# Performance work log

Measured on AMD Instinct MI355X. Metric: run time of the kernel, lower is better.

## Reference

```python
import jax, jax.numpy as jnp
import numpy as np

N_USERS, N_ITEMS, DIM = 50000, 25000, 128
E_H, E_R = 600000, 1000000
N_LAYERS = 2


def setup_inputs() -> dict:
    key = jax.random.key(0)
    ks = jax.random.split(key, 20)
    nrm = lambda k, s: jax.random.normal(k, s, jnp.float32) * 0.05
    inp = {
        "u_emb": nrm(ks[0], (N_USERS, DIM)),
        "i_emb": nrm(ks[1], (N_ITEMS, DIM)),
        "gating_W": nrm(ks[2], (4, DIM, DIM)),
        "gating_b": jnp.zeros((4, DIM), jnp.float32),
        "attention": nrm(ks[3], (DIM,)),
        "attention_mat": nrm(ks[4], (DIM, DIM)),
    }
    for i, name in enumerate(["Hs", "Hj", "Hp"]):
        inp[name + "_row"] = jax.random.randint(ks[5 + 2 * i], (E_H,), 0, N_USERS, jnp.int32)
        inp[name + "_col"] = jax.random.randint(ks[6 + 2 * i], (E_H,), 0, N_USERS, jnp.int32)
        inp[name + "_val"] = jax.random.uniform(ks[11 + i], (E_H,), jnp.float32)
    inp["R_row"] = jax.random.randint(ks[14], (E_R,), 0, N_USERS, jnp.int32)
    inp["R_col"] = jax.random.randint(ks[15], (E_R,), 0, N_ITEMS, jnp.int32)
    inp["R_val"] = jnp.ones((E_R,), jnp.float32)
    return inp


def spmm(row, col, val, X, n_out):
    # sparse (n_out x n_in) @ dense (n_in x d), COO edge list form
    return jax.ops.segment_sum(val[:, None] * X[col], row, num_segments=n_out)


def l2norm(x):
    return x * jax.lax.rsqrt(jnp.maximum(jnp.sum(x * x, axis=1, keepdims=True), 1e-12))


def reference(u_emb, i_emb, gating_W, gating_b, attention, attention_mat,
              Hs_row, Hs_col, Hs_val, Hj_row, Hj_col, Hj_val,
              Hp_row, Hp_col, Hp_val, R_row, R_col, R_val):
    gate = lambda e, c: e * jax.nn.sigmoid(e @ gating_W[c] + gating_b[c])

    def chan_att(cs):
        # per-channel attention score: sum_d a_d * (E_c @ W_att)_d  -> [N, C]
        w = jnp.stack([jnp.sum(attention * (c @ attention_mat), axis=1) for c in cs], axis=1)
        s = jax.nn.softmax(w, axis=1)
        mixed = sum(s[:, k:k + 1] * cs[k] for k in range(len(cs)))
        return mixed, s

    H = [(Hs_row, Hs_col, Hs_val), (Hj_row, Hj_col, Hj_val), (Hp_row, Hp_col, Hp_val)]
    cur = [gate(u_emb, c) for c in range(3)]        # channel user embeddings
    cur_s = gate(u_emb, 3)                          # simple-gated user embeddings
    cur_i = i_emb
    all_c = [[cur[k]] for k in range(3)]
    all_i = [cur_i]
    all_s = [cur_s]
    for _ in range(N_LAYERS):
        mixed = chan_att(cur)[0] + cur_s / 2
        for k in range(3):
            r, c, v = H[k]
            cur[k] = spmm(r, c, v, cur[k], N_USERS)
            all_c[k].append(l2norm(cur[k]))
        new_item = spmm(R_col, R_row, R_val, mixed, N_ITEMS)   # R^T @ mixed
        all_i.append(l2norm(new_item))
        cur_s = spmm(R_row, R_col, R_val, cur_i, N_USERS)      # R @ item
        all_s.append(l2norm(cur_s))
        cur_i = new_item
    fc = [sum(all_c[k]) for k in range(3)]
    final_user = chan_att(fc)[0] + sum(all_s) / 2
    final_item = sum(all_i)
    return jnp.concatenate([final_user, final_item], axis=0)  # [N_USERS+N_ITEMS, DIM]
```

## Files before the change

kernel.cpp:

```cpp
#include <hip/hip_runtime.h>
#include <cstddef>
#include <cstdint>

#define NU 50000
#define NI 25000
#define DIMN 128
#define EH 600000
#define ER 1000000

typedef unsigned int u32;
typedef unsigned long long u64;
typedef unsigned char u8;
typedef __attribute__((ext_vector_type(8))) short short8;
typedef __attribute__((ext_vector_type(16))) float float16;

__device__ __forceinline__ float wave_sum64(float v) {
#pragma unroll
  for (int m = 32; m >= 1; m >>= 1) v += __shfl_xor(v, m, 64);
  return v;
}

__device__ __forceinline__ u32 pack_bf16x2(float a, float b) {
  u32 ua = __float_as_uint(a), ub = __float_as_uint(b);
  ua = (ua + 0x7fffu + ((ua >> 16) & 1u)) >> 16;
  ub = (ub + 0x7fffu + ((ub >> 16) & 1u)) >> 16;
  return ua | (ub << 16);
}
__device__ __forceinline__ u32 bf16_hi(float v) {
  u32 u = __float_as_uint(v);
  u = (u + 0x7fffu + ((u >> 16) & 1u)) & 0xffff0000u;
  return u;
}
__device__ __forceinline__ float blo(u32 p) { return __uint_as_float(p << 16); }
__device__ __forceinline__ float bhi(u32 p) { return __uint_as_float(p & 0xffff0000u); }

struct Graphs {
  const int* row[5];
  const int* col[5];
  const float* val[5];
};

__device__ __forceinline__ int g_E(int z) {
  const int E[5] = {EH, EH, EH, ER, ER};
  return E[z];
}

#define NBKU 196
#define TOTB (5 * NBKU)
#define CAPH 3584
#define CAPR 5632
#define CAPT 5632
#define ECAP 4315136
#define FCAP 5760
#define CHUNK 2048

#define BSH 293
#define BSR 489
#define B1SCAT (3 * BSH + 2 * BSR)
#define B1PREP 18879
#define B2FINE TOTB
#define B2GATE (782 * 4)

__device__ __forceinline__ int capstart(int z, int b) {
  const int base[5] = {0, 702464, 1404928, 2107392, 3211264};
  const int cap[5] = {CAPH, CAPH, CAPH, CAPR, CAPT};
  return base[z] + b * cap[z];
}

__global__ __launch_bounds__(256) void k_build1(Graphs g, int* __restrict__ bcnt,
                                                u32* __restrict__ epb, u8* __restrict__ erb,
                                                const float* __restrict__ U,
                                                u32* __restrict__ UP16,
                                                const float* __restrict__ IE,
                                                u32* __restrict__ IE16,
                                                const float* __restrict__ W,
                                                u32* __restrict__ W16,
                                                const float* __restrict__ attm,
                                                const float* __restrict__ att,
                                                float* __restrict__ attv) {
  int b = blockIdx.x;
  if (b < B1SCAT) {
    int z, cb;
    if (b < 3 * BSH) {
      z = b / BSH;
      cb = b - z * BSH;
    } else {
      int r = b - 3 * BSH;
      z = 3 + r / BSR;
      cb = r - (z - 3) * BSR;
    }
    int E = g_E(z);
    int sh = (z == 4) ? 7 : 8;
    int mask = (1 << sh) - 1;
    __shared__ int hist[2][NBKU], basel[NBKU], curl[2][NBKU], h0s[NBKU];
    for (int i = threadIdx.x; i < NBKU; i += 256) {
      hist[0][i] = 0;
      hist[1][i] = 0;
      curl[0][i] = 0;
      curl[1][i] = 0;
    }
    __syncthreads();
    const int* __restrict__ row = g.row[z];
    const int* __restrict__ col = g.col[z];
    const float* __restrict__ val = g.val[z];
    int e0 = cb * CHUNK + threadIdx.x * 8;
    int half = threadIdx.x >> 7;
    int r[8];
    u32 pay[8];
    bool ok[8];
    if (e0 + 8 <= E) {
      int4 ra = *(const int4*)(row + e0);
      int4 rb = *(const int4*)(row + e0 + 4);
      int4 ca = *(const int4*)(col + e0);
      int4 cbv = *(const int4*)(col + e0 + 4);
      r[0] = ra.x; r[1] = ra.y; r[2] = ra.z; r[3] = ra.w;
      r[4] = rb.x; r[5] = rb.y; r[6] = rb.z; r[7] = rb.w;
      pay[0] = (u32)ca.x; pay[1] = (u32)ca.y; pay[2] = (u32)ca.z; pay[3] = (u32)ca.w;
      pay[4] = (u32)cbv.x; pay[5] = (u32)cbv.y; pay[6] = (u32)cbv.z; pay[7] = (u32)cbv.w;
#pragma unroll
      for (int k = 0; k < 8; ++k) ok[k] = true;
      if (z < 3) {
        float4 va = *(const float4*)(val + e0);
        float4 vb = *(const float4*)(val + e0 + 4);
        pay[0] |= bf16_hi(va.x); pay[1] |= bf16_hi(va.y);
        pay[2] |= bf16_hi(va.z); pay[3] |= bf16_hi(va.w);
        pay[4] |= bf16_hi(vb.x); pay[5] |= bf16_hi(vb.y);
        pay[6] |= bf16_hi(vb.z); pay[7] |= bf16_hi(vb.w);
      }
    } else {
#pragma unroll
      for (int k = 0; k < 8; ++k) {
        int e = e0 + k;
        ok[k] = e < E;
        r[k] = ok[k] ? row[e] : 0;
        pay[k] = ok[k] ? (u32)col[e] : 0u;
        if (z < 3 && ok[k]) pay[k] |= bf16_hi(val[e]);
      }
    }
#pragma unroll
    for (int k = 0; k < 8; ++k)
      if (ok[k]) atomicAdd(&hist[half][r[k] >> sh], 1);
    __syncthreads();
    for (int i = threadIdx.x; i < NBKU; i += 256) {
      int h0 = hist[0][i];
      int tot = h0 + hist[1][i];
      h0s[i] = h0;
      if (tot) basel[i] = capstart(z, i) + atomicAdd(&bcnt[z * NBKU + i], tot);
    }
    __syncthreads();
#pragma unroll
    for (int k = 0; k < 8; ++k)
      if (ok[k]) {
        int bb = r[k] >> sh;
        int rank = atomicAdd(&curl[half][bb], 1);
        int pos = basel[bb] + (half ? h0s[bb] : 0) + rank;
        epb[pos] = pay[k];
        erb[pos] = (u8)(r[k] & mask);
      }
    return;
  }
  int b2 = b - B1SCAT;
  if (b2 < 12500) {
    int i = b2 * 256 + threadIdx.x;
    float2 v = ((const float2*)U)[i];
    UP16[i] = pack_bf16x2(v.x, v.y);
  } else if (b2 < 18750) {
    int i = (b2 - 12500) * 256 + threadIdx.x;
    float2 v = ((const float2*)IE)[i];
    IE16[i] = pack_bf16x2(v.x, v.y);
  } else if (b2 < 18878) {
    int i = (b2 - 18750) * 256 + threadIdx.x;
    int col = i & 127, k2 = (i >> 7) & 63, c = i >> 13;
    const float* Wc = W + (size_t)c * DIMN * DIMN;
    W16[i] = pack_bf16x2(Wc[(size_t)(2 * k2) * DIMN + col], Wc[(size_t)(2 * k2 + 1) * DIMN + col]);
  } else {
    int e = threadIdx.x;
    if (e < 128) {
      float s = 0.f;
      for (int d = 0; d < DIMN; ++d) s += attm[e * DIMN + d] * att[d];
      attv[e] = s;
    }
  }
}

struct FineLds {
  int cnt[256];
  int scn[256];
  int curl[256];
  u32 buf[FCAP];
};
struct GateLds {
  u32 ldsP[64 * 65];
};

__global__ __launch_bounds__(256) void k_build2(u32* __restrict__ epb, const u8* __restrict__ erb,
                                                const int* __restrict__ bcnt,
                                                int* __restrict__ ptr2,
                                                const u32* __restrict__ UP16,
                                                const u32* __restrict__ W16,
                                                const float* __restrict__ B, u32* S16,
                                                u32* G016, u32* G116, u32* G216) {
  __shared__ __align__(16) union {
    FineLds f;
    GateLds g;
  } sh;
  int b = blockIdx.x;
  int t = threadIdx.x;
  if (b < B2FINE) {
    int z = b / NBKU, bb = b - z * NBKU;
    int shf = (z == 4) ? 7 : 8;
    int mask = (1 << shf) - 1;
    const int poffs2[5] = {0, 100000, 200000, 300000, 400000};
    const int nz[5] = {NU, NU, NU, NU, NI};
    int s = capstart(z, bb);
    int n = bcnt[z * NBKU + bb];
    FineLds& L = sh.f;
    L.cnt[t] = 0;
    L.curl[t] = 0;
    __syncthreads();
    int n4 = n >> 2;
    for (int i = t; i < n4; i += 256) {
      u32 r4 = *(const u32*)(erb + s + 4 * i);
      atomicAdd(&L.cnt[r4 & 255u], 1);
      atomicAdd(&L.cnt[(r4 >> 8) & 255u], 1);
      atomicAdd(&L.cnt[(r4 >> 16) & 255u], 1);
      atomicAdd(&L.cnt[r4 >> 24], 1);
    }
    for (int i = 4 * n4 + t; i < n; i += 256) atomicAdd(&L.cnt[erb[s + i]], 1);
    __syncthreads();
    int v = L.cnt[t];
    L.scn[t] = v;
    __syncthreads();
    for (int o = 1; o < 256; o <<= 1) {
      int x = (t >= o) ? L.scn[t - o] : 0;
      __syncthreads();
      L.scn[t] += x;
      __syncthreads();
    }
    int excl = L.scn[t] - v;
    __syncthreads();
    L.scn[t] = excl;
    int rg = (bb << shf) + t;
    if (t <= mask && rg < nz[z]) {
      ptr2[poffs2[z] + 2 * rg] = s + excl;
      ptr2[poffs2[z] + 2 * rg + 1] = s + excl + v;
    }
    __syncthreads();
    for (int i = t; i < n4; i += 256) {
      u32 r4 = *(const u32*)(erb + s + 4 * i);
      uint4 p4 = *(const uint4*)(epb + s + 4 * i);
      int r0 = (int)(r4 & 255u);
      int k0 = atomicAdd(&L.curl[r0], 1);
      L.buf[L.scn[r0] + k0] = p4.x;
      int r1 = (int)((r4 >> 8) & 255u);
      int k1 = atomicAdd(&L.curl[r1], 1);
      L.buf[L.scn[r1] + k1] = p4.y;
      int r2 = (int)((r4 >> 16) & 255u);
      int k2 = atomicAdd(&L.curl[r2], 1);
      L.buf[L.scn[r2] + k2] = p4.z;
      int r3 = (int)(r4 >> 24);
      int k3 = atomicAdd(&L.curl[r3], 1);
      L.buf[L.scn[r3] + k3] = p4.w;
    }
    for (int i = 4 * n4 + t; i < n; i += 256) {
      int r = erb[s + i];
      int rank = atomicAdd(&L.curl[r], 1);
      L.buf[L.scn[r] + rank] = epb[s + i];
    }
    __syncthreads();
    for (int i = t; i < n4; i += 256) ((uint4*)(epb + s))[i] = ((const uint4*)L.buf)[i];
    for (int i = 4 * n4 + t; i < n; i += 256) epb[s + i] = L.buf[i];
    return;
  }
  int gb = b - B2FINE;
  int c = gb / 782;
  int r0 = (gb - c * 782) * 64;
  const u32* __restrict__ Wc = W16 + (size_t)c * (64 * 128);
  int w = t >> 6, lane = t & 63;
  int ln = lane & 31, h = lane >> 5;
  int rh = w & 1, mh = w >> 1;
  u32* ldsP = sh.g.ldsP;

  int rowl = rh * 32 + ln;
  int rg = r0 + rowl;
  int rc = (rg < NU) ? rg : (NU - 1);

  float16 acc[2];
#pragma unroll
  for (int m = 0; m < 2; ++m)
#pragma unroll
    for (int q = 0; q < 16; ++q) acc[m][q] = 0.f;

  const u32* __restrict__ urow = UP16 + (size_t)rc * 64;
#pragma unroll
  for (int kk = 0; kk < 8; ++kk) {
    int kw = kk * 8 + 4 * h;
    union {
      u32 u[4];
      short8 s;
    } bf;
#pragma unroll
    for (int j = 0; j < 4; ++j) bf.u[j] = urow[kw + j];
#pragma unroll
    for (int m = 0; m < 2; ++m) {
      union {
        u32 u[4];
        short8 s;
      } af;
      int col = 64 * mh + 32 * m + ln;
#pragma unroll
      for (int j = 0; j < 4; ++j) af.u[j] = Wc[(size_t)(kw + j) * DIMN + col];
      acc[m] = __builtin_amdgcn_mfma_f32_32x32x16_bf16(af.s, bf.s, acc[m], 0, 0, 0);
    }
  }
#pragma unroll
  for (int m = 0; m < 2; ++m)
#pragma unroll
    for (int q = 0; q < 16; q += 2) {
      int cw = 32 * mh + 16 * m + ((q & 3) >> 1) + 4 * (q >> 2) + 2 * h;
      ldsP[rowl * 65 + cw] = pack_bf16x2(acc[m][q], acc[m][q + 1]);
    }
  __syncthreads();

  int colw = t & 63, rloc = t >> 6;
  float bx = B[c * DIMN + 2 * colw], by = B[c * DIMN + 2 * colw + 1];
  u32* dst = (c == 0) ? G016 : (c == 1) ? G116 : (c == 2) ? G216 : S16;
#pragma unroll
  for (int i = 0; i < 16; ++i) {
    int row = i * 4 + rloc;
    int rg2 = r0 + row;
    if (rg2 >= NU) continue;
    u32 p = ldsP[row * 65 + colw];
    u32 uu = UP16[(size_t)rg2 * 64 + colw];
    float sx = 1.f / (1.f + __expf(-(blo(p) + bx)));
    float sy = 1.f / (1.f + __expf(-(bhi(p) + by)));
    dst[(size_t)rg2 * 64 + colw] = pack_bf16x2(blo(uu) * sx, bhi(uu) * sy);
  }
}

struct Job {
  const int* ptr2;
  const u32* X16;
  u32* Y16;
  float* ACCF;
  u32* ACC16;
  const u32* AINIT16;
  const float* AINITF;
  int nrows;
};

template <bool UNIT>
__device__ __forceinline__ void spmm_run(const u32* __restrict__ ep, const Job& jb) {
  int w = blockIdx.x * 4 + __builtin_amdgcn_readfirstlane(threadIdx.x >> 6);
  int lane = threadIdx.x & 63;
  if (w >= jb.nrows) return;
  const int2 pp = ((const int2*)jb.ptr2)[w];
  int s = __builtin_amdgcn_readfirstlane(pp.x);
  int t = __builtin_amdgcn_readfirstlane(pp.y);
  const char* __restrict__ Xb = (const char*)jb.X16;
  u32 lo4 = (u32)(lane << 2);
  float ax = 0.f, ay = 0.f;
  int e = s;
  for (; e + 8 <= t; e += 8) {
    u32 off[8];
    float vv[8];
#pragma unroll
    for (int k = 0; k < 8; ++k) {
      u32 q = ep[e + k];
      if (UNIT) {
        off[k] = (q << 8) | lo4;
      } else {
        off[k] = ((q & 0xffffu) << 8) | lo4;
        vv[k] = bhi(q);
      }
    }
    u32 p[8];
#pragma unroll
    for (int k = 0; k < 8; ++k) p[k] = *(const u32*)(Xb + off[k]);
#pragma unroll
    for (int k = 0; k < 8; ++k) {
      if (UNIT) {
        ax += blo(p[k]);
        ay += bhi(p[k]);
      } else {
        ax += vv[k] * blo(p[k]);
        ay += vv[k] * bhi(p[k]);
      }
    }
  }
  for (; e + 4 <= t; e += 4) {
    u32 off[4];
    float vv[4];
#pragma unroll
    for (int k = 0; k < 4; ++k) {
      u32 q = ep[e + k];
      if (UNIT) {
        off[k] = (q << 8) | lo4;
      } else {
        off[k] = ((q & 0xffffu) << 8) | lo4;
        vv[k] = bhi(q);
      }
    }
    u32 p[4];
#pragma unroll
    for (int k = 0; k < 4; ++k) p[k] = *(const u32*)(Xb + off[k]);
#pragma unroll
    for (int k = 0; k < 4; ++k) {
      if (UNIT) {
        ax += blo(p[k]);
        ay += bhi(p[k]);
      } else {
        ax += vv[k] * blo(p[k]);
        ay += vv[k] * bhi(p[k]);
      }
    }
  }
  for (; e < t; ++e) {
    u32 q = ep[e];
    u32 off;
    float v = 1.f;
    if (UNIT) {
      off = (q << 8) | lo4;
    } else {
      off = ((q & 0xffffu) << 8) | lo4;
      v = bhi(q);
    }
    u32 p = *(const u32*)(Xb + off);
    ax += v * blo(p);
    ay += v * bhi(p);
  }
  size_t b64 = (size_t)w * 64 + lane;
  if (jb.ACCF) {
    float ss = wave_sum64(ax * ax + ay * ay);
    float rs = rsqrtf(fmaxf(ss, 1e-12f));
    if (jb.Y16) jb.Y16[b64] = pack_bf16x2(ax, ay);
    float2 o;
    if (jb.AINITF)
      o = *(const float2*)(jb.AINITF + 2 * b64);
    else
      o = *(const float2*)(jb.ACCF + 2 * b64);
    o.x += ax * rs;
    o.y += ay * rs;
    *(float2*)(jb.ACCF + 2 * b64) = o;
  } else if (jb.ACC16) {
    float ss = wave_sum64(ax * ax + ay * ay);
    float rs = rsqrtf(fmaxf(ss, 1e-12f));
    u32 p = jb.AINIT16 ? jb.AINIT16[b64] : jb.ACC16[b64];
    float ox = blo(p) + ax * rs, oy = bhi(p) + ay * rs;
    if (jb.Y16) jb.Y16[b64] = pack_bf16x2(ax, ay);
    jb.ACC16[b64] = pack_bf16x2(ox, oy);
  } else if (jb.Y16) {
    jb.Y16[b64] = pack_bf16x2(ax, ay);
  }
}

__global__ __launch_bounds__(256) void k_spmm5(const u32* __restrict__ ep, Job j0, Job j1,
                                               Job j2, Job j3, Job j4) {
  int y = blockIdx.y;
  if (y < 2) {
    Job jb = (y == 0) ? j0 : j1;
    spmm_run<true>(ep, jb);
  } else {
    Job jb = (y == 2) ? j2 : (y == 3) ? j3 : j4;
    spmm_run<false>(ep, jb);
  }
}

template <bool OUT16>
__global__ __launch_bounds__(256) void k_mix(const u32* __restrict__ c0_,
                                             const u32* __restrict__ c1_,
                                             const u32* __restrict__ c2_,
                                             const u32* __restrict__ sp_,
                                             const float* __restrict__ attv, float* outf,
                                             u32* out16, int nrows) {
  int w = blockIdx.x * 4 + __builtin_amdgcn_readfirstlane(threadIdx.x >> 6);
  int lane = threadIdx.x & 63;
  if (w >= nrows) return;
  size_t b64 = (size_t)w * 64 + lane;
  u32 p0 = c0_[b64], p1 = c1_[b64], p2 = c2_[b64];
  float2 x0 = make_float2(blo(p0), bhi(p0));
  float2 x1 = make_float2(blo(p1), bhi(p1));
  float2 x2 = make_float2(blo(p2), bhi(p2));
  float2 av = *(const float2*)(attv + lane * 2);
  float w0 = wave_sum64(x0.x * av.x + x0.y * av.y);
  float w1 = wave_sum64(x1.x * av.x + x1.y * av.y);
  float w2 = wave_sum64(x2.x * av.x + x2.y * av.y);
  float m = fmaxf(w0, fmaxf(w1, w2));
  float e0 = __expf(w0 - m), e1 = __expf(w1 - m), e2 = __expf(w2 - m);
  float inv = 1.f / (e0 + e1 + e2);
  float s0 = e0 * inv, s1 = e1 * inv, s2 = e2 * inv;
  u32 ps = sp_[b64];
  float ox = s0 * x0.x + s1 * x1.x + s2 * x2.x + 0.5f * blo(ps);
  float oy = s0 * x0.y + s1 * x1.y + s2 * x2.y + 0.5f * bhi(ps);
  if (OUT16)
    out16[b64] = pack_bf16x2(ox, oy);
  else
    *(float2*)(outf + 2 * b64) = make_float2(ox, oy);
}

extern "C" void kernel_launch(void* const* d_in, const int* in_sizes, int n_in, void* d_out,
                              int out_size, void* d_ws, size_t ws_size, hipStream_t stream) {
  const float* u_emb = (const float*)d_in[0];
  const float* i_emb = (const float*)d_in[1];
  const float* gW = (const float*)d_in[2];
  const float* gB = (const float*)d_in[3];
  const float* att = (const float*)d_in[4];
  const float* attm = (const float*)d_in[5];
  Graphs g;
  g.row[0] = (const int*)d_in[6];
  g.col[0] = (const int*)d_in[7];
  g.val[0] = (const float*)d_in[8];
  g.row[1] = (const int*)d_in[9];
  g.col[1] = (const int*)d_in[10];
  g.val[1] = (const float*)d_in[11];
  g.row[2] = (const int*)d_in[12];
  g.col[2] = (const int*)d_in[13];
  g.val[2] = (const float*)d_in[14];
  g.row[3] = (const int*)d_in[15];
  g.col[3] = (const int*)d_in[16];
  g.val[3] = (const float*)d_in[17];
  g.row[4] = (const int*)d_in[16];
  g.col[4] = (const int*)d_in[15];
  g.val[4] = (const float*)d_in[17];

  const size_t U = (size_t)NU * DIMN, U64 = (size_t)NU * 64, I64 = (size_t)NI * 64;
  u32* G016 = (u32*)d_ws;
  u32* G116 = G016 + U64;
  u32* G216 = G116 + U64;
  u32* C1016 = G216 + U64;
  u32* C1116 = C1016 + U64;
  u32* C1216 = C1116 + U64;
  u32* GS016 = C1216 + U64;
  u32* GS116 = GS016 + U64;
  u32* GS216 = GS116 + U64;
  u32* MIX16 = GS216 + U64;
  u32* S16 = MIX16 + U64;
  u32* SACC = S16 + U64;
  u32* I116 = SACC + U64;
  u32* IE16 = I116 + I64;
  u32* UP16 = IE16 + I64;
  u32* W16 = UP16 + U64;
  float* attv = (float*)(W16 + 32768);
  int* ptr2 = (int*)(attv + DIMN);
  int* bcnt = ptr2 + 450000;
  uintptr_t a0 = ((uintptr_t)(bcnt + 984) + 15u) & ~(uintptr_t)15;
  u32* epb = (u32*)a0;
  u8* erb = (u8*)(epb + ECAP);
  float* out_u = (float*)d_out;
  float* out_i = out_u + U;

  const int GRID_U = (NU + 3) / 4;
  const int po1 = 100000, po2 = 200000, po3 = 300000, po4 = 400000;

  hipMemsetAsync(bcnt, 0, TOTB * sizeof(int), stream);
  hipLaunchKernelGGL(k_build1, dim3(B1SCAT + B1PREP), dim3(256), 0, stream, g, bcnt, epb, erb,
                     u_emb, UP16, i_emb, IE16, gW, W16, attm, att, attv);
  hipLaunchKernelGGL(k_build2, dim3(B2FINE + B2GATE), dim3(256), 0, stream, epb, erb, bcnt, ptr2,
                     UP16, W16, gB, S16, G016, G116, G216);

  hipLaunchKernelGGL((k_mix<true>), dim3(GRID_U), dim3(256), 0, stream, G016, G116, G216, S16,
                     attv, (float*)nullptr, MIX16, NU);
  {
    Job j0 = {ptr2 + po3, IE16, S16, nullptr, SACC, S16, nullptr, NU};
    Job j1 = {ptr2 + po4, MIX16, I116, out_i, nullptr, nullptr, i_emb, NI};
    Job j2 = {ptr2, G016, C1016, nullptr, GS016, G016, nullptr, NU};
    Job j3 = {ptr2 + po1, G116, C1116, nullptr, GS116, G116, nullptr, NU};
    Job j4 = {ptr2 + po2, G216, C1216, nullptr, GS216, G216, nullptr, NU};
    hipLaunchKernelGGL(k_spmm5, dim3(GRID_U, 5), dim3(256), 0, stream, epb, j0, j1, j2, j3, j4);
  }

  hipLaunchKernelGGL((k_mix<true>), dim3(GRID_U), dim3(256), 0, stream, C1016, C1116, C1216, S16,
                     attv, (float*)nullptr, MIX16, NU);
  {
    Job j0 = {ptr2 + po3, I116, nullptr, nullptr, SACC, nullptr, nullptr, NU};
    Job j1 = {ptr2 + po4, MIX16, nullptr, out_i, nullptr, nullptr, nullptr, NI};
    Job j2 = {ptr2, C1016, nullptr, nullptr, GS016, nullptr, nullptr, NU};
    Job j3 = {ptr2 + po1, C1116, nullptr, nullptr, GS116, nullptr, nullptr, NU};
    Job j4 = {ptr2 + po2, C1216, nullptr, nullptr, GS216, nullptr, nullptr, NU};
    hipLaunchKernelGGL(k_spmm5, dim3(GRID_U, 5), dim3(256), 0, stream, epb, j0, j1, j2, j3, j4);
  }

  hipLaunchKernelGGL((k_mix<false>), dim3(GRID_U), dim3(256), 0, stream, GS016, GS116, GS216,
                     SACC, attv, out_u, (u32*)nullptr, NU);
}
```

Baseline: 495.2 us.

## Fuse four gating channels and channel-attention mix into build2 with vectorized bf16 prep

```diff
diff --git a/kernel.cpp b/kernel.cpp
--- a/kernel.cpp
+++ b/kernel.cpp
@@ -57,9 +57,12 @@
 #define BSH 293
 #define BSR 489
 #define B1SCAT (3 * BSH + 2 * BSR)
-#define B1PREP 18879
+#define PU 3125
+#define PIE 1563
+#define PW 128
+#define B1PREP (PU + PIE + PW + 1)
 #define B2FINE TOTB
-#define B2GATE (782 * 4)
+#define B2GATE 782
 
 __device__ __forceinline__ int capstart(int z, int b) {
   const int base[5] = {0, 702464, 1404928, 2107392, 3211264};
@@ -160,16 +163,30 @@
     return;
   }
   int b2 = b - B1SCAT;
-  if (b2 < 12500) {
+  if (b2 < PU) {
     int i = b2 * 256 + threadIdx.x;
-    float2 v = ((const float2*)U)[i];
-    UP16[i] = pack_bf16x2(v.x, v.y);
-  } else if (b2 < 18750) {
-    int i = (b2 - 12500) * 256 + threadIdx.x;
-    float2 v = ((const float2*)IE)[i];
-    IE16[i] = pack_bf16x2(v.x, v.y);
-  } else if (b2 < 18878) {
-    int i = (b2 - 18750) * 256 + threadIdx.x;
+    float4 a = ((const float4*)U)[2 * i];
+    float4 c = ((const float4*)U)[2 * i + 1];
+    uint4 o;
+    o.x = pack_bf16x2(a.x, a.y);
+    o.y = pack_bf16x2(a.z, a.w);
+    o.z = pack_bf16x2(c.x, c.y);
+    o.w = pack_bf16x2(c.z, c.w);
+    ((uint4*)UP16)[i] = o;
+  } else if (b2 < PU + PIE) {
+    int i = (b2 - PU) * 256 + threadIdx.x;
+    if (i < (NI * DIMN) / 8) {
+      float4 a = ((const float4*)IE)[2 * i];
+      float4 c = ((const float4*)IE)[2 * i + 1];
+      uint4 o;
+      o.x = pack_bf16x2(a.x, a.y);
+      o.y = pack_bf16x2(a.z, a.w);
+      o.z = pack_bf16x2(c.x, c.y);
+      o.w = pack_bf16x2(c.z, c.w);
+      ((uint4*)IE16)[i] = o;
+    }
+  } else if (b2 < PU + PIE + PW) {
+    int i = (b2 - PU - PIE) * 256 + threadIdx.x;
     int col = i & 127, k2 = (i >> 7) & 63, c = i >> 13;
     const float* Wc = W + (size_t)c * DIMN * DIMN;
     W16[i] = pack_bf16x2(Wc[(size_t)(2 * k2) * DIMN + col], Wc[(size_t)(2 * k2 + 1) * DIMN + col]);
@@ -184,22 +201,27 @@
 }
 
 struct FineLds {
-  int cnt[256];
-  int scn[256];
-  int curl[256];
+  int cnt[1024];
+  int scn[1024];
+  int curl[1024];
   u32 buf[FCAP];
 };
 struct GateLds {
-  u32 ldsP[64 * 65];
+  u32 ldsP[4][64 * 64];
 };
 
-__global__ __launch_bounds__(256) void k_build2(u32* __restrict__ epb, const u8* __restrict__ erb,
-                                                const int* __restrict__ bcnt,
-                                                int* __restrict__ ptr2,
-                                                const u32* __restrict__ UP16,
-                                                const u32* __restrict__ W16,
-                                                const float* __restrict__ B, u32* S16,
-                                                u32* G016, u32* G116, u32* G216) {
+__device__ __forceinline__ int gsw(int row, int col) { return row * 64 + (col ^ (row & 31)); }
+
+__global__ __launch_bounds__(1024) void k_build2(u32* __restrict__ epb,
+                                                 const u8* __restrict__ erb,
+                                                 const int* __restrict__ bcnt,
+                                                 int* __restrict__ ptr2,
+                                                 const u32* __restrict__ UP16,
+                                                 const u32* __restrict__ W16,
+                                                 const float* __restrict__ B,
+                                                 const float* __restrict__ attv, u32* S16,
+                                                 u32* G016, u32* G116, u32* G216,
+                                                 u32* MIX16) {
   __shared__ __align__(16) union {
     FineLds f;
     GateLds g;
@@ -219,14 +241,14 @@
     L.curl[t] = 0;
     __syncthreads();
     int n4 = n >> 2;
-    for (int i = t; i < n4; i += 256) {
+    for (int i = t; i < n4; i += 1024) {
       u32 r4 = *(const u32*)(erb + s + 4 * i);
       atomicAdd(&L.cnt[r4 & 255u], 1);
       atomicAdd(&L.cnt[(r4 >> 8) & 255u], 1);
       atomicAdd(&L.cnt[(r4 >> 16) & 255u], 1);
       atomicAdd(&L.cnt[r4 >> 24], 1);
     }
-    for (int i = 4 * n4 + t; i < n; i += 256) atomicAdd(&L.cnt[erb[s + i]], 1);
+    for (int i = 4 * n4 + t; i < n; i += 1024) atomicAdd(&L.cnt[erb[s + i]], 1);
     __syncthreads();
     int v = L.cnt[t];
     L.scn[t] = v;
@@ -246,7 +268,7 @@
       ptr2[poffs2[z] + 2 * rg + 1] = s + excl + v;
     }
     __syncthreads();
-    for (int i = t; i < n4; i += 256) {
+    for (int i = t; i < n4; i += 1024) {
       u32 r4 = *(const u32*)(erb + s + 4 * i);
       uint4 p4 = *(const uint4*)(epb + s + 4 * i);
       int r0 = (int)(r4 & 255u);
@@ -262,24 +284,26 @@
       int k3 = atomicAdd(&L.curl[r3], 1);
       L.buf[L.scn[r3] + k3] = p4.w;
     }
-    for (int i = 4 * n4 + t; i < n; i += 256) {
+    for (int i = 4 * n4 + t; i < n; i += 1024) {
       int r = erb[s + i];
       int rank = atomicAdd(&L.curl[r], 1);
       L.buf[L.scn[r] + rank] = epb[s + i];
     }
     __syncthreads();
-    for (int i = t; i < n4; i += 256) ((uint4*)(epb + s))[i] = ((const uint4*)L.buf)[i];
-    for (int i = 4 * n4 + t; i < n; i += 256) epb[s + i] = L.buf[i];
+    for (int i = t; i < n4; i += 1024) ((uint4*)(epb + s))[i] = ((const uint4*)L.buf)[i];
+    for (int i = 4 * n4 + t; i < n; i += 1024) epb[s + i] = L.buf[i];
     return;
   }
   int gb = b - B2FINE;
-  int c = gb / 782;
-  int r0 = (gb - c * 782) * 64;
-  const u32* __restrict__ Wc = W16 + (size_t)c * (64 * 128);
-  int w = t >> 6, lane = t & 63;
+  int r0 = gb * 64;
+  int wv = t >> 6;
+  int c = wv >> 2;
+  int w = wv & 3;
+  int lane = t & 63;
   int ln = lane & 31, h = lane >> 5;
   int rh = w & 1, mh = w >> 1;
-  u32* ldsP = sh.g.ldsP;
+  const u32* __restrict__ Wc = W16 + (size_t)c * (64 * 128);
+  u32* ldsP = sh.g.ldsP[c];
 
   int rowl = rh * 32 + ln;
   int rg = r0 + rowl;
@@ -318,23 +342,53 @@
 #pragma unroll
     for (int q = 0; q < 16; q += 2) {
       int cw = 32 * mh + 16 * m + ((q & 3) >> 1) + 4 * (q >> 2) + 2 * h;
-      ldsP[rowl * 65 + cw] = pack_bf16x2(acc[m][q], acc[m][q + 1]);
+      ldsP[gsw(rowl, cw)] = pack_bf16x2(acc[m][q], acc[m][q + 1]);
     }
   __syncthreads();
 
-  int colw = t & 63, rloc = t >> 6;
-  float bx = B[c * DIMN + 2 * colw], by = B[c * DIMN + 2 * colw + 1];
-  u32* dst = (c == 0) ? G016 : (c == 1) ? G116 : (c == 2) ? G216 : S16;
-#pragma unroll
-  for (int i = 0; i < 16; ++i) {
-    int row = i * 4 + rloc;
+  int colw = lane;
+  float2 av = *(const float2*)(attv + 2 * colw);
+  float2 b0 = ((const float2*)B)[colw];
+  float2 b1 = ((const float2*)B)[64 + colw];
+  float2 b2 = ((const float2*)B)[128 + colw];
+  float2 b3 = ((const float2*)B)[192 + colw];
+#pragma unroll
+  for (int i = 0; i < 4; ++i) {
+    int row = wv + i * 16;
     int rg2 = r0 + row;
     if (rg2 >= NU) continue;
-    u32 p = ldsP[row * 65 + colw];
-    u32 uu = UP16[(size_t)rg2 * 64 + colw];
-    float sx = 1.f / (1.f + __expf(-(blo(p) + bx)));
-    float sy = 1.f / (1.f + __expf(-(bhi(p) + by)));
-    dst[(size_t)rg2 * 64 + colw] = pack_bf16x2(blo(uu) * sx, bhi(uu) * sy);
+    size_t o64 = (size_t)rg2 * 64 + colw;
+    u32 uu = UP16[o64];
+    float ux = blo(uu), uy = bhi(uu);
+    u32 p0 = sh.g.ldsP[0][gsw(row, colw)];
+    u32 p1 = sh.g.ldsP[1][gsw(row, colw)];
+    u32 p2 = sh.g.ldsP[2][gsw(row, colw)];
+    u32 p3 = sh.g.ldsP[3][gsw(row, colw)];
+    u32 g0 = pack_bf16x2(ux / (1.f + __expf(-(blo(p0) + b0.x))),
+                         uy / (1.f + __expf(-(bhi(p0) + b0.y))));
+    u32 g1 = pack_bf16x2(ux / (1.f + __expf(-(blo(p1) + b1.x))),
+                         uy / (1.f + __expf(-(bhi(p1) + b1.y))));
+    u32 g2 = pack_bf16x2(ux / (1.f + __expf(-(blo(p2) + b2.x))),
+                         uy / (1.f + __expf(-(bhi(p2) + b2.y))));
+    u32 g3 = pack_bf16x2(ux / (1.f + __expf(-(blo(p3) + b3.x))),
+                         uy / (1.f + __expf(-(bhi(p3) + b3.y))));
+    G016[o64] = g0;
+    G116[o64] = g1;
+    G216[o64] = g2;
+    S16[o64] = g3;
+    float x0x = blo(g0), x0y = bhi(g0);
+    float x1x = blo(g1), x1y = bhi(g1);
+    float x2x = blo(g2), x2y = bhi(g2);
+    float w0 = wave_sum64(x0x * av.x + x0y * av.y);
+    float w1 = wave_sum64(x1x * av.x + x1y * av.y);
+    float w2 = wave_sum64(x2x * av.x + x2y * av.y);
+    float m = fmaxf(w0, fmaxf(w1, w2));
+    float e0 = __expf(w0 - m), e1 = __expf(w1 - m), e2 = __expf(w2 - m);
+    float inv = 1.f / (e0 + e1 + e2);
+    float s0 = e0 * inv, s1 = e1 * inv, s2 = e2 * inv;
+    float ox = s0 * x0x + s1 * x1x + s2 * x2x + 0.5f * blo(g3);
+    float oy = s0 * x0y + s1 * x1y + s2 * x2y + 0.5f * bhi(g3);
+    MIX16[o64] = pack_bf16x2(ox, oy);
   }
 }
 
@@ -555,11 +609,9 @@
   hipMemsetAsync(bcnt, 0, TOTB * sizeof(int), stream);
   hipLaunchKernelGGL(k_build1, dim3(B1SCAT + B1PREP), dim3(256), 0, stream, g, bcnt, epb, erb,
                      u_emb, UP16, i_emb, IE16, gW, W16, attm, att, attv);
-  hipLaunchKernelGGL(k_build2, dim3(B2FINE + B2GATE), dim3(256), 0, stream, epb, erb, bcnt, ptr2,
-                     UP16, W16, gB, S16, G016, G116, G216);
-
-  hipLaunchKernelGGL((k_mix<true>), dim3(GRID_U), dim3(256), 0, stream, G016, G116, G216, S16,
-                     attv, (float*)nullptr, MIX16, NU);
+  hipLaunchKernelGGL(k_build2, dim3(B2FINE + B2GATE), dim3(1024), 0, stream, epb, erb, bcnt,
+                     ptr2, UP16, W16, gB, attv, S16, G016, G116, G216, MIX16);
+
   {
     Job j0 = {ptr2 + po3, IE16, S16, nullptr, SACC, S16, nullptr, NU};
     Job j1 = {ptr2 + po4, MIX16, I116, out_i, nullptr, nullptr, i_emb, NI};
```

After: 491.8 us, median of 2. About the same (-0.7%).
